# Kernel optimization log

Measured on AMD Instinct MI355X. Metric: run time of the kernel, lower is better.

## Reference

```python
import jax, jax.numpy as jnp
import numpy as np

EMBED_DIM = 1024
NUM_HEADS = 16
HEAD_DIM = EMBED_DIM // NUM_HEADS
T, B = 2048, 8


def setup_inputs() -> dict:
    key = jax.random.key(0)
    ks = jax.random.split(key, 7)
    s = 1.0 / np.sqrt(EMBED_DIM)
    return {
        "query": jax.random.normal(ks[0], (T, B, EMBED_DIM), jnp.float32),
        "key": jax.random.normal(ks[1], (T, B, EMBED_DIM), jnp.float32),
        "value": jax.random.normal(ks[2], (T, B, EMBED_DIM), jnp.float32),
        "w_qkv": jax.random.uniform(ks[3], (3 * EMBED_DIM, EMBED_DIM), jnp.float32, -s, s),
        "b_qkv": jnp.zeros((3 * EMBED_DIM,), jnp.float32),
        "w_out": jax.random.uniform(ks[4], (EMBED_DIM, EMBED_DIM), jnp.float32, -s, s),
        "b_out": jnp.zeros((EMBED_DIM,), jnp.float32),
    }


def reference(query, key, value, w_qkv, b_qkv, w_out, b_out):
    # key/value are only used for src_len in the original; src_len == tgt_len here.
    tgt_len, bsz, _ = query.shape
    BH = bsz * NUM_HEADS
    qkv = jnp.einsum("tbe,fe->tbf", query, w_qkv) + b_qkv  # [T, B, 3E]
    q, k, v = jnp.split(qkv, 3, axis=-1)
    q = q.reshape(tgt_len, BH, HEAD_DIM)
    k = k.reshape(tgt_len, BH, HEAD_DIM)
    v = v.reshape(tgt_len, BH, HEAD_DIM)
    # L2-normalize q and k along head_dim (no eps, matching torch .norm division)
    q = q / jnp.linalg.norm(q, axis=-1, keepdims=True)
    k = k / jnp.linalg.norm(k, axis=-1, keepdims=True)
    # NOTE: matmul batches over dim0 = tgt_len, mixing across the B*H axis (faithful to source)
    scores = jnp.einsum("tad,tbd->tab", q, k) / np.sqrt(HEAD_DIM)  # [T, BH, BH]
    probs = jax.nn.softmax(scores, axis=-1)
    ws = jnp.einsum("tab,tbd->tad", probs, v)  # [T, BH, hd]
    ws = ws.reshape(tgt_len, bsz, NUM_HEADS, HEAD_DIM)
    ws = jnp.transpose(ws, (1, 0, 2, 3)).reshape(bsz, tgt_len, EMBED_DIM)
    out = jnp.einsum("bte,fe->btf", ws, w_out) + b_out  # [B, T, E]
    return out
```

## Files before the change

### kernel.cpp

```cpp
#include <hip/hip_runtime.h>
#include <hip/hip_bf16.h>
#include <stdint.h>


typedef __attribute__((ext_vector_type(8))) short short8;
typedef __attribute__((ext_vector_type(4))) float floatx4;

__device__ __forceinline__ float bf2f(short s) {
  union { unsigned u; float f; } v;
  v.u = ((unsigned)(unsigned short)s) << 16;
  return v.f;
}
__device__ __forceinline__ short f2bf(float x) {
  union { float f; unsigned u; } v; v.f = x;
  unsigned u = v.u;
  unsigned r = (u + 0x7fffu + ((u >> 16) & 1u)) >> 16;
  return (short)r;
}
__device__ __forceinline__ short8 pack_bf8(float4 lo, float4 hi) {
  short8 r;
  r[0] = f2bf(lo.x); r[1] = f2bf(lo.y); r[2] = f2bf(lo.z); r[3] = f2bf(lo.w);
  r[4] = f2bf(hi.x); r[5] = f2bf(hi.y); r[6] = f2bf(hi.z); r[7] = f2bf(hi.w);
  return r;
}

__device__ __forceinline__ void gl2lds16(const short* g, short* l) {
  __builtin_amdgcn_global_load_lds(
      (const __attribute__((address_space(1))) void*)g,
      (__attribute__((address_space(3))) void*)l, 16, 0, 0);
}

__global__ __launch_bounds__(256)
void cvt_bf16(const float* __restrict__ in, short* __restrict__ out, int n8) {
  const int i = blockIdx.x * 256 + threadIdx.x;
  if (i < n8) {
    float4 a = ((const float4*)in)[2 * i];
    float4 b = ((const float4*)in)[2 * i + 1];
    ((short8*)out)[i] = pack_bf8(a, b);
  }
}


#define DO_MFMA(BI, BJ)                                                      \
  __builtin_amdgcn_s_setprio(1);                                             \
  _Pragma("unroll")                                                          \
  for (int k = 0; k < 2; ++k)                                                \
    _Pragma("unroll")                                                        \
    for (int i = 0; i < 4; ++i)                                              \
      _Pragma("unroll")                                                      \
      for (int j = 0; j < 2; ++j)                                            \
        acc[(BI) + i][(BJ) + j] = __builtin_amdgcn_mfma_f32_16x16x32_bf16(   \
            af[i][k], bfv[(BJ) + j][k], acc[(BI) + i][(BJ) + j], 0, 0, 0);   \
  __builtin_amdgcn_s_setprio(0);

#define READ_A(SRC, MH)                                                      \
  _Pragma("unroll")                                                          \
  for (int i = 0; i < 4; ++i) {                                              \
    af[i][0] = *(const short8*)((SRC) + aRow + (MH) * 4096 + i * 1024 + kOff0); \
    af[i][1] = *(const short8*)((SRC) + aRow + (MH) * 4096 + i * 1024 + kOff1); \
  }

#define READ_B(SRC, NH)                                                      \
  _Pragma("unroll")                                                          \
  for (int j = 0; j < 2; ++j) {                                              \
    bfv[(NH) * 2 + j][0] = *(const short8*)((SRC) + bRow + (NH) * 2048 + j * 1024 + kOff0); \
    bfv[(NH) * 2 + j][1] = *(const short8*)((SRC) + bRow + (NH) * 2048 + j * 1024 + kOff1); \
  }

#define FENCE asm volatile("" ::: "memory")
#define BAR_LGK FENCE; __builtin_amdgcn_s_barrier(); FENCE
#define BAR_END FENCE; __builtin_amdgcn_s_barrier(); FENCE
#define WAIT_VM(N)                                                           \
  asm volatile("s_waitcnt vmcnt(" #N ")" ::: "memory");                      \
  __builtin_amdgcn_sched_barrier(0)

template <int EPI>
__global__ __launch_bounds__(512, 2)
void gemm_bf(const short* __restrict__ A, const short* __restrict__ W,
             const float* __restrict__ bias, void* __restrict__ o0,
             void* __restrict__ o1, void* __restrict__ o2, int K,
             int rowbase, int tsh) {
  __shared__ __align__(16) short lds[2][2][16384];

  const int tid  = threadIdx.x;
  const int lane = tid & 63, wave = tid >> 6;
  const int l15  = lane & 15, quad = lane >> 4;
  const int wm   = wave >> 2, wn = wave & 3;

  const int gx   = gridDim.x;
  const int nwg  = gx * gridDim.y;
  const int orig = blockIdx.y * gx + blockIdx.x;
  const int qq = nwg >> 3, rr = nwg & 7;
  const int xcd = orig & 7, off = orig >> 3;
  const int wgid = (xcd < rr ? xcd * (qq + 1) : rr * (qq + 1) + (xcd - rr) * qq) + off;
  const int m0 = (wgid / gx) * 256, n0 = (wgid % gx) * 256;

  const int rl0 = tid >> 3;
  const int ic0 = (tid & 7) << 4;
  const int sc  = ic0 ^ ((rl0 & 7) << 4);
  const short* Ag = A + (size_t)(m0 + rl0) * K + (sc >> 1);
  const short* Wg = W + (size_t)(n0 + rl0) * K + (sc >> 1);

  const int NT = K >> 6;

  auto stageA = [&](int buf, int h, int t) {
    const short* g = Ag + (size_t)(h * 128) * K + t * 64;
    short* d = &lds[buf][0][h * 8192 + tid * 8];
    gl2lds16(g, d);
    gl2lds16(g + (size_t)64 * K, d + 4096);
  };
  auto stageB = [&](int buf, int h, int t) {
    const short* g = Wg + (size_t)(h * 128) * K + t * 64;
    short* d = &lds[buf][1][h * 8192 + tid * 8];
    gl2lds16(g, d);
    gl2lds16(g + (size_t)64 * K, d + 4096);
  };

  const int xsw   = (l15 & 7) << 4;
  const int aRow  = (wm * 128 + l15) * 64;
  const int bRow  = (wn * 64 + l15) * 64;
  const int kOff0 = ((quad * 16) ^ xsw) >> 1;
  const int kOff1 = ((64 + quad * 16) ^ xsw) >> 1;

  floatx4 acc[8][4] = {};

  stageA(0, 0, 0); stageA(0, 1, 0); stageB(0, 0, 0); stageB(0, 1, 0);
  stageB(1, 0, 1); stageA(1, 0, 1);
  WAIT_VM(4);
  BAR_END;

  short8 af[4][2], bfv[4][2];
  const short* const A0 = lds[0][0]; const short* const B0 = lds[0][1];
  const short* const A1 = lds[1][0]; const short* const B1 = lds[1][1];

  const int NI = NT >> 1;
  for (int it = 0; it < NI; ++it) {
    const bool st = (it + 1 < NI);
    const int to = 2 * it + 1, ta = 2 * it + 2, tb = 2 * it + 3;

    READ_A(A0, 0); READ_B(B0, 0);
    stageA(1, 1, to);
    BAR_LGK;
    DO_MFMA(0, 0);
    BAR_END;

    READ_B(B0, 1);
    stageB(1, 1, to);
    BAR_LGK;
    DO_MFMA(0, 2);
    BAR_END;

    READ_A(A0, 1);
    if (st) stageB(0, 0, ta);
    BAR_LGK;
    DO_MFMA(4, 0);
    BAR_END;

    if (st) stageA(0, 0, ta);
    DO_MFMA(4, 2);
    if (st) { WAIT_VM(4); }
    else    { WAIT_VM(0); }
    BAR_END;

    READ_A(A1, 0); READ_B(B1, 0);
    if (st) stageA(0, 1, ta);
    BAR_LGK;
    DO_MFMA(0, 0);
    BAR_END;

    READ_B(B1, 1);
    if (st) stageB(0, 1, ta);
    BAR_LGK;
    DO_MFMA(0, 2);
    BAR_END;

    READ_A(A1, 1);
    if (st) stageB(1, 0, tb);
    BAR_LGK;
    DO_MFMA(4, 0);
    BAR_END;

    if (st) stageA(1, 0, tb);
    DO_MFMA(4, 2);
    if (st) { WAIT_VM(4); }
    BAR_END;
  }

  if constexpr (EPI == 0) {
    float bv[4]; int ee[4]; short* op[4];
#pragma unroll
    for (int j = 0; j < 4; ++j) {
      const int n = n0 + wn * 64 + j * 16 + l15;
      bv[j] = bias[n];
      const int which = n >> 10;
      ee[j] = n & 1023;
      op[j] = (which == 0) ? (short*)o0 : ((which == 1) ? (short*)o1 : (short*)o2);
    }
#pragma unroll
    for (int i = 0; i < 8; ++i)
#pragma unroll
      for (int r = 0; r < 4; ++r) {
        const int mloc = m0 + wm * 128 + i * 16 + quad * 4 + r;
        const size_t rowoff = (size_t)mloc * 1024;
#pragma unroll
        for (int j = 0; j < 4; ++j)
          op[j][rowoff + ee[j]] = f2bf(acc[i][j][r] + bv[j]);
      }
  } else {
    float bv[4]; int nn[4];
#pragma unroll
    for (int j = 0; j < 4; ++j) {
      nn[j] = n0 + wn * 64 + j * 16 + l15;
      bv[j] = bias[nn[j]];
    }
#pragma unroll
    for (int i = 0; i < 8; ++i)
#pragma unroll
      for (int r = 0; r < 4; ++r) {
        const int mloc = m0 + wm * 128 + i * 16 + quad * 4 + r;
        const int g = ((mloc >> tsh) << 11) + rowbase + (mloc & ((1 << tsh) - 1));
        const size_t rowoff = (size_t)g * 1024;
#pragma unroll
        for (int j = 0; j < 4; ++j)
          ((float*)o0)[rowoff + nn[j]] = acc[i][j][r] + bv[j];
      }
  }
}

__global__ __launch_bounds__(256)
void attn_kernel(const short* __restrict__ qb, const short* __restrict__ kb,
                 const short* __restrict__ vb, short* __restrict__ wsb, int tch) {
  __shared__ __align__(16) char smem[55296];
  short* qs  = (short*)smem;
  short* ks  = (short*)(smem + 18432);
  short* Ps  = (short*)smem;
  short* vt  = (short*)(smem + 36864);
  float* rsq = (float*)(smem + 54272);
  float* rsk = rsq + 128;

  const int tp   = blockIdx.x;
  const int tid  = threadIdx.x;
  const int lane = tid & 63, wave = tid >> 6;
  const int l15  = lane & 15, quad = lane >> 4;
  const size_t base = (size_t)tp * 8192;

#pragma unroll
  for (int it = 0; it < 4; it++) {
    const int c = tid + it * 256;
    const int row = c >> 3, c8 = (c & 7) * 8;
    uint4 qv = *(const uint4*)(qb + base + row * 64 + c8);
    uint4 kv = *(const uint4*)(kb + base + row * 64 + c8);
    *(uint4*)(qs + row * 72 + c8) = qv;
    *(uint4*)(ks + row * 72 + c8) = kv;
    short tmp[8];
    *(uint4*)tmp = *(const uint4*)(vb + base + row * 64 + c8);
#pragma unroll
    for (int j = 0; j < 8; j++) vt[(c8 + j) * 136 + row] = tmp[j];
  }
  __syncthreads();

  {
    const short* src = (tid < 128) ? qs : ks;
    const int r = tid & 127;
    const short8* rp = (const short8*)(src + r * 72);
    float s = 0.f;
#pragma unroll
    for (int k8 = 0; k8 < 8; k8++) {
      short8 v = rp[k8];
#pragma unroll
      for (int j = 0; j < 8; j++) { float x = bf2f(v[j]); s += x * x; }
    }
    ((tid < 128) ? rsq : rsk)[r] = rsqrtf(s);
  }
  __syncthreads();

  const int wm = wave >> 1, wn = wave & 1;
  floatx4 acc[4][4] = {};
#pragma unroll
  for (int kk = 0; kk < 64; kk += 32) {
    short8 af[4], bfv[4];
#pragma unroll
    for (int i = 0; i < 4; i++)
      af[i] = *(const short8*)(qs + (wm * 64 + i * 16 + l15) * 72 + kk + quad * 8);
#pragma unroll
    for (int j = 0; j < 4; j++)
      bfv[j] = *(const short8*)(ks + (wn * 64 + j * 16 + l15) * 72 + kk + quad * 8);
#pragma unroll
    for (int i = 0; i < 4; i++)
#pragma unroll
      for (int j = 0; j < 4; j++)
        acc[i][j] = __builtin_amdgcn_mfma_f32_16x16x32_bf16(af[i], bfv[j], acc[i][j], 0, 0, 0);
  }
  __syncthreads();

#pragma unroll
  for (int i = 0; i < 4; i++)
#pragma unroll
    for (int j = 0; j < 4; j++)
#pragma unroll
      for (int r = 0; r < 4; r++) {
        const int a    = wm * 64 + i * 16 + quad * 4 + r;
        const int bcol = wn * 64 + j * 16 + l15;
        Ps[a * 136 + bcol] = f2bf(acc[i][j][r] * rsq[a] * rsk[bcol] * 0.125f);
      }
  __syncthreads();

  {
    const int r = tid >> 1, h = tid & 1;
    short8* rp = (short8*)(Ps + r * 136 + h * 64);
    short8 v[8];
    float mx = -1e30f;
#pragma unroll
    for (int k8 = 0; k8 < 8; k8++) {
      v[k8] = rp[k8];
#pragma unroll
      for (int j = 0; j < 8; j++) mx = fmaxf(mx, bf2f(v[k8][j]));
    }
    mx = fmaxf(mx, __shfl_xor(mx, 1, 64));
    float sum = 0.f;
#pragma unroll
    for (int k8 = 0; k8 < 8; k8++) {
      short8 o;
#pragma unroll
      for (int j = 0; j < 8; j++) {
        float p = __expf(bf2f(v[k8][j]) - mx);
        sum += p;
        o[j] = f2bf(p);
      }
      rp[k8] = o;
    }
    sum += __shfl_xor(sum, 1, 64);
    if (h == 0) rsq[r] = 1.0f / sum;
  }
  __syncthreads();

  floatx4 acc2[2][4] = {};
#pragma unroll
  for (int kb2 = 0; kb2 < 128; kb2 += 32) {
    short8 af[2], bfv[4];
#pragma unroll
    for (int ti = 0; ti < 2; ti++)
      af[ti] = *(const short8*)(Ps + (wave * 32 + ti * 16 + l15) * 136 + kb2 + quad * 8);
#pragma unroll
    for (int tj = 0; tj < 4; tj++)
      bfv[tj] = *(const short8*)(vt + (tj * 16 + l15) * 136 + kb2 + quad * 8);
#pragma unroll
    for (int ti = 0; ti < 2; ti++)
#pragma unroll
      for (int tj = 0; tj < 4; tj++)
        acc2[ti][tj] = __builtin_amdgcn_mfma_f32_16x16x32_bf16(af[ti], bfv[tj], acc2[ti][tj], 0, 0, 0);
  }

#pragma unroll
  for (int ti = 0; ti < 2; ti++)
#pragma unroll
    for (int tj = 0; tj < 4; tj++)
#pragma unroll
      for (int r = 0; r < 4; r++) {
        const int a = wave * 32 + ti * 16 + quad * 4 + r;
        const int d = tj * 16 + l15;
        const float v = acc2[ti][tj][r] * rsq[a];
        const int bz = a >> 4, h = a & 15;
        wsb[((size_t)bz * tch + tp) * 1024 + h * 64 + d] = f2bf(v);
      }
}

extern "C" void kernel_launch(void* const* d_in, const int* in_sizes, int n_in,
                              void* d_out, int out_size, void* d_ws, size_t ws_size,
                              hipStream_t stream) {
  const float* query = (const float*)d_in[0];
  const float* w_qkv = (const float*)d_in[3];
  const float* b_qkv = (const float*)d_in[4];
  const float* w_out = (const float*)d_in[5];
  const float* b_out = (const float*)d_in[6];
  float* out = (float*)d_out;

  int C = 64;
  for (int c = 1; c <= 64; c <<= 1) {
    if ((size_t)(8388608 + 134217728 / c) <= ws_size) { C = c; break; }
  }
  const int Mc  = 16384 / C;
  const int TCH = 2048 / C;
  int tsh = 0; while ((1 << tsh) < TCH) tsh++;

  short* wqkvb = (short*)d_ws;
  short* woutb = wqkvb + 3145728;
  short* qbuf  = woutb + 1048576;
  short* kbuf  = qbuf + (size_t)Mc * 1024;
  short* vbuf  = kbuf + (size_t)Mc * 1024;
  short* wsb   = vbuf + (size_t)Mc * 1024;

  cvt_bf16<<<3145728 / 8 / 256, 256, 0, stream>>>(w_qkv, wqkvb, 3145728 / 8);
  cvt_bf16<<<1048576 / 8 / 256, 256, 0, stream>>>(w_out, woutb, 1048576 / 8);

  for (int c = 0; c < C; c++) {
    const int n8 = Mc * 1024 / 8;
    cvt_bf16<<<(n8 + 255) / 256, 256, 0, stream>>>(query + (size_t)c * Mc * 1024, wsb, n8);
    gemm_bf<0><<<dim3(12, Mc / 256), 512, 0, stream>>>(
        wsb, wqkvb, b_qkv, qbuf, kbuf, vbuf, 1024, 0, 0);
    attn_kernel<<<TCH, 256, 0, stream>>>(qbuf, kbuf, vbuf, wsb, TCH);
    gemm_bf<1><<<dim3(4, Mc / 256), 512, 0, stream>>>(
        wsb, woutb, b_out, out, nullptr, nullptr, 1024, c * TCH, tsh);
  }
}
```

Measured before the change: 358.2 us.

## Restructure GEMM main loop to hold full B fragments and stage whole tiles

Reworks the double-buffered bf16 GEMM mainloop. The B fragments for all four N-subtiles now stay in registers, and two A fragment sets are kept, so each LDS tile is read once per k-step rather than re-reading B halves. Global-to-LDS staging now issues whole A/B tiles in two phases, with vmcnt waits of 8 instead of interleaving half-tiles across phases. This cuts LDS read traffic and simplifies the schedule, at the cost of more VGPRs under launch_bounds(512,2) and a coarser prefetch overlap.

```diff
diff --git a/kernel.cpp b/kernel.cpp
--- a/kernel.cpp
+++ b/kernel.cpp
@@ -41,7 +41,7 @@
 }
 
 
-#define DO_MFMA(BI, BJ)                                                      \
+#define DO_MFMA(BI, BJ, AF, BF)                                              \
   __builtin_amdgcn_s_setprio(1);                                             \
   _Pragma("unroll")                                                          \
   for (int k = 0; k < 2; ++k)                                                \
@@ -50,26 +50,25 @@
       _Pragma("unroll")                                                      \
       for (int j = 0; j < 2; ++j)                                            \
         acc[(BI) + i][(BJ) + j] = __builtin_amdgcn_mfma_f32_16x16x32_bf16(   \
-            af[i][k], bfv[(BJ) + j][k], acc[(BI) + i][(BJ) + j], 0, 0, 0);   \
+            (AF)[i][k], (BF)[j][k], acc[(BI) + i][(BJ) + j], 0, 0, 0);       \
   __builtin_amdgcn_s_setprio(0);
 
-#define READ_A(SRC, MH)                                                      \
+#define READ_AF(DST, SRC, MH)                                                \
   _Pragma("unroll")                                                          \
   for (int i = 0; i < 4; ++i) {                                              \
-    af[i][0] = *(const short8*)((SRC) + aRow + (MH) * 4096 + i * 1024 + kOff0); \
-    af[i][1] = *(const short8*)((SRC) + aRow + (MH) * 4096 + i * 1024 + kOff1); \
-  }
-
-#define READ_B(SRC, NH)                                                      \
+    DST[i][0] = *(const short8*)((SRC) + aRow + (MH) * 4096 + i * 1024 + kOff0); \
+    DST[i][1] = *(const short8*)((SRC) + aRow + (MH) * 4096 + i * 1024 + kOff1); \
+  }
+
+#define READ_BF(DST, SRC, OFF)                                               \
   _Pragma("unroll")                                                          \
   for (int j = 0; j < 2; ++j) {                                              \
-    bfv[(NH) * 2 + j][0] = *(const short8*)((SRC) + bRow + (NH) * 2048 + j * 1024 + kOff0); \
-    bfv[(NH) * 2 + j][1] = *(const short8*)((SRC) + bRow + (NH) * 2048 + j * 1024 + kOff1); \
+    DST[j][0] = *(const short8*)((SRC) + bRow + (OFF) + j * 1024 + kOff0);   \
+    DST[j][1] = *(const short8*)((SRC) + bRow + (OFF) + j * 1024 + kOff1);   \
   }
 
 #define FENCE asm volatile("" ::: "memory")
-#define BAR_LGK FENCE; __builtin_amdgcn_s_barrier(); FENCE
-#define BAR_END FENCE; __builtin_amdgcn_s_barrier(); FENCE
+#define BAR FENCE; __builtin_amdgcn_s_barrier(); FENCE
 #define WAIT_VM(N)                                                           \
   asm volatile("s_waitcnt vmcnt(" #N ")" ::: "memory");                      \
   __builtin_amdgcn_sched_barrier(0)
@@ -125,65 +124,56 @@
   floatx4 acc[8][4] = {};
 
   stageA(0, 0, 0); stageA(0, 1, 0); stageB(0, 0, 0); stageB(0, 1, 0);
-  stageB(1, 0, 1); stageA(1, 0, 1);
-  WAIT_VM(4);
-  BAR_END;
-
-  short8 af[4][2], bfv[4][2];
+  stageB(1, 0, 1); stageB(1, 1, 1); stageA(1, 0, 1); stageA(1, 1, 1);
+  WAIT_VM(8);
+  BAR;
+
+  short8 afA[4][2], afB[4][2], bf01[2][2], bf23[2][2];
   const short* const A0 = lds[0][0]; const short* const B0 = lds[0][1];
   const short* const A1 = lds[1][0]; const short* const B1 = lds[1][1];
 
   const int NI = NT >> 1;
   for (int it = 0; it < NI; ++it) {
     const bool st = (it + 1 < NI);
-    const int to = 2 * it + 1, ta = 2 * it + 2, tb = 2 * it + 3;
-
-    READ_A(A0, 0); READ_B(B0, 0);
-    stageA(1, 1, to);
-    BAR_LGK;
-    DO_MFMA(0, 0);
-    BAR_END;
-
-    READ_B(B0, 1);
-    stageB(1, 1, to);
-    BAR_LGK;
-    DO_MFMA(0, 2);
-    BAR_END;
-
-    READ_A(A0, 1);
-    if (st) stageB(0, 0, ta);
-    BAR_LGK;
-    DO_MFMA(4, 0);
-    BAR_END;
-
-    if (st) stageA(0, 0, ta);
-    DO_MFMA(4, 2);
-    if (st) { WAIT_VM(4); }
-    else    { WAIT_VM(0); }
-    BAR_END;
-
-    READ_A(A1, 0); READ_B(B1, 0);
-    if (st) stageA(0, 1, ta);
-    BAR_LGK;
-    DO_MFMA(0, 0);
-    BAR_END;
-
-    READ_B(B1, 1);
-    if (st) stageB(0, 1, ta);
-    BAR_LGK;
-    DO_MFMA(0, 2);
-    BAR_END;
-
-    READ_A(A1, 1);
-    if (st) stageB(1, 0, tb);
-    BAR_LGK;
-    DO_MFMA(4, 0);
-    BAR_END;
-
-    if (st) stageA(1, 0, tb);
-    DO_MFMA(4, 2);
-    if (st) { WAIT_VM(4); }
-    BAR_END;
+    const int e2 = 2 * it + 2, o3 = 2 * it + 3;
+
+    READ_AF(afA, A0, 0); READ_BF(bf01, B0, 0); READ_BF(bf23, B0, 2048);
+    BAR;
+    DO_MFMA(0, 0, afA, bf01);
+    BAR;
+
+    READ_AF(afB, A0, 1);
+    BAR;
+    DO_MFMA(0, 2, afA, bf23);
+    BAR;
+
+    if (st) { stageB(0, 0, e2); stageB(0, 1, e2); }
+    DO_MFMA(4, 2, afB, bf23);
+    BAR;
+
+    if (st) { stageA(0, 0, e2); stageA(0, 1, e2); }
+    DO_MFMA(4, 0, afB, bf01);
+    if (st) { WAIT_VM(8); } else { WAIT_VM(0); }
+    BAR;
+
+    READ_AF(afA, A1, 0); READ_BF(bf01, B1, 0); READ_BF(bf23, B1, 2048);
+    BAR;
+    DO_MFMA(0, 0, afA, bf01);
+    BAR;
+
+    READ_AF(afB, A1, 1);
+    BAR;
+    DO_MFMA(0, 2, afA, bf23);
+    BAR;
+
+    if (st) { stageB(1, 0, o3); stageB(1, 1, o3); }
+    DO_MFMA(4, 2, afB, bf23);
+    BAR;
+
+    if (st) { stageA(1, 0, o3); stageA(1, 1, o3); }
+    DO_MFMA(4, 0, afB, bf01);
+    if (st) { WAIT_VM(8); }
+    BAR;
   }
 
   if constexpr (EPI == 0) {
```

Measured after the change: 367.0 us. 1.02x slower.
